# Kernel optimization log

Measured on AMD Instinct MI355X. Metric: run time of the kernel, lower is better.

## Reference

```python
import jax, jax.numpy as jnp
import numpy as np

N_MICS = 8
REF_MIC = 0
DIAG_LOAD = 1e-5
PI_ITERS = 30  # power-iteration steps for principal eigenvector of Phi_nn^-1 Phi_ss


def setup_inputs() -> dict:
    key = jax.random.key(0)
    k1, k2, k3, k4 = jax.random.split(key, 4)
    B, M, F, T = 8, N_MICS, 257, 2000
    return {
        "spec_re": jax.random.normal(k1, (B, M, F, T), dtype=jnp.float32),
        "spec_im": jax.random.normal(k2, (B, M, F, T), dtype=jnp.float32),
        "speech_mask": jax.random.uniform(k3, (B, F, T), dtype=jnp.float32),
        "noise_mask": jax.random.uniform(k4, (B, F, T), dtype=jnp.float32),
    }


def _mvdr(spec_re, spec_im, speech_mask, noise_mask):
    # (B, M, F, T) complex STFT -> (B, F, M, T) for per-(batch, freq) processing
    Y = (spec_re + 1j * spec_im).astype(jnp.complex64)
    Y = jnp.transpose(Y, (0, 2, 1, 3))  # (B, F, M, T)
    M = Y.shape[2]

    def masked_cov(mask):  # mask: (B, F, T) real
        msum = mask.sum(-1) + 1e-8                       # (B, F)
        Yw = Y * mask[:, :, None, :]                      # (B, F, M, T)
        Phi = jnp.einsum('bfmt,bfnt->bfmn', Yw, Y.conj())  # (B, F, M, M)
        return Phi / msum[..., None, None]

    Phi_ss = masked_cov(speech_mask)
    eye = jnp.eye(M, dtype=jnp.complex64)
    Phi_nn = masked_cov(noise_mask) + DIAG_LOAD * eye

    Phi_nn_inv = jnp.linalg.inv(Phi_nn)                   # batched (B, F, M, M)
    G = jnp.einsum('bfmn,bfnk->bfmk', Phi_nn_inv, Phi_ss)

    # Principal eigenvector of G via power iteration (G has real, nonnegative
    # eigenvalues since it is similar to a Hermitian-PSD generalized pencil),
    # matching torch.linalg.eig + argmax(eigenvalues.real) up to scale.
    v = jnp.ones(G.shape[:-1], dtype=jnp.complex64)       # (B, F, M)
    for _ in range(PI_ITERS):
        v = jnp.einsum('bfmn,bfn->bfm', G, v)
        v = v / (jnp.linalg.norm(v, axis=-1, keepdims=True) + 1e-12)

    # Relative transfer function normalized to reference mic (removes scale)
    rtf = v / (v[..., REF_MIC:REF_MIC + 1] + 1e-8)        # (B, F, M)

    d = jnp.einsum('bfmn,bfn->bfm', Phi_nn_inv, rtf)      # Phi_nn^-1 rtf
    denom = jnp.einsum('bfm,bfm->bf', rtf.conj(), d).real + 1e-8
    w = d / denom[..., None]                              # (B, F, M) MVDR weights

    enhanced = jnp.einsum('bfm,bfmt->bft', w.conj(), Y)   # (B, F, T) complex
    return enhanced


def reference(spec_re, spec_im, speech_mask, noise_mask):
    return _mvdr(spec_re, spec_im, speech_mask, noise_mask)
```

## Files before the change

### kernel.cpp

```cpp
#include <hip/hip_runtime.h>

#define B_DIM 8
#define M_MICS 8
#define F_DIM 257
#define T_DIM 2000


#define PAIR_ACC(mq, nq, k)                                             \
    {                                                                   \
        const float pr = yr[mq][u] * yr[nq][u] + yi[mq][u] * yi[nq][u]; \
        const float pi = yi[mq][u] * yr[nq][u] - yr[mq][u] * yi[nq][u]; \
        acc[(k) + 0] += msv[u] * pr;                                    \
        acc[(k) + 1] += msv[u] * pi;                                    \
        acc[(k) + 2] += mnv[u] * pr;                                    \
        acc[(k) + 3] += mnv[u] * pi;                                    \
    }

__launch_bounds__(256, 4)
__global__ void mvdr_fused(const float* __restrict__ sre, const float* __restrict__ sim,
                           const float* __restrict__ smask, const float* __restrict__ nmask,
                           float* __restrict__ out, int out_mode)
{
    const int f = blockIdx.x, b = blockIdx.y, tid = threadIdx.x;
    const int h = tid >> 6, l = tid & 63;

    __shared__ float sG[4][34];
    __shared__ float sW[16];

    const size_t mrow = (size_t)F_DIM * T_DIM;
    const size_t base_bf = ((size_t)(b * M_MICS) * F_DIM + f) * T_DIM;
    const size_t mbase   = ((size_t)b * F_DIM + f) * T_DIM;

    float acc[34];
#pragma unroll
    for (int i = 0; i < 34; ++i) acc[i] = 0.f;

#pragma unroll 1
    for (int it = 0; it < 16; ++it) {
        const int t0 = 2 * l + 128 * it;
        if (t0 < T_DIM) {
            float yr[8][2], yi[8][2];
#pragma unroll
            for (int m = 0; m < 8; ++m) {
                const float2 vr = *reinterpret_cast<const float2*>(sre + base_bf + (size_t)m * mrow + t0);
                const float2 vi = *reinterpret_cast<const float2*>(sim + base_bf + (size_t)m * mrow + t0);
                yr[m][0] = vr.x; yr[m][1] = vr.y;
                yi[m][0] = vi.x; yi[m][1] = vi.y;
            }
            const float2 ms2 = *reinterpret_cast<const float2*>(smask + mbase + t0);
            const float2 mn2 = *reinterpret_cast<const float2*>(nmask + mbase + t0);
            const float msv[2] = { ms2.x, ms2.y };
            const float mnv[2] = { mn2.x, mn2.y };

            if (h == 0) {
#pragma unroll
                for (int u = 0; u < 2; ++u) {
                    acc[0] += msv[u];
                    acc[1] += mnv[u];
#pragma unroll
                    for (int m = 0; m < 8; ++m) {
                        const float pd = yr[m][u] * yr[m][u] + yi[m][u] * yi[m][u];
                        acc[2 + m]  += msv[u] * pd;
                        acc[10 + m] += mnv[u] * pd;
                    }
                    PAIR_ACC(0, 1, 18) PAIR_ACC(0, 2, 22) PAIR_ACC(0, 3, 26) PAIR_ACC(0, 4, 30)
                }
            } else if (h == 1) {
#pragma unroll
                for (int u = 0; u < 2; ++u) {
                    PAIR_ACC(0, 5, 0)  PAIR_ACC(0, 6, 4)  PAIR_ACC(0, 7, 8)  PAIR_ACC(1, 2, 12)
                    PAIR_ACC(1, 3, 16) PAIR_ACC(1, 4, 20) PAIR_ACC(1, 5, 24) PAIR_ACC(1, 6, 28)
                }
            } else if (h == 2) {
#pragma unroll
                for (int u = 0; u < 2; ++u) {
                    PAIR_ACC(1, 7, 0)  PAIR_ACC(2, 3, 4)  PAIR_ACC(2, 4, 8)  PAIR_ACC(2, 5, 12)
                    PAIR_ACC(2, 6, 16) PAIR_ACC(2, 7, 20) PAIR_ACC(3, 4, 24) PAIR_ACC(3, 5, 28)
                }
            } else {
#pragma unroll
                for (int u = 0; u < 2; ++u) {
                    PAIR_ACC(3, 6, 0)  PAIR_ACC(3, 7, 4)  PAIR_ACC(4, 5, 8)  PAIR_ACC(4, 6, 12)
                    PAIR_ACC(4, 7, 16) PAIR_ACC(5, 6, 20) PAIR_ACC(5, 7, 24) PAIR_ACC(6, 7, 28)
                }
            }
        }
    }

#pragma unroll
    for (int i = 0; i < 34; ++i) {
        acc[i] += __shfl_xor(acc[i], 1, 64);
        acc[i] += __shfl_xor(acc[i], 2, 64);
        acc[i] += __shfl_xor(acc[i], 4, 64);
        acc[i] += __shfl_xor(acc[i], 8, 64);
        acc[i] += __shfl_xor(acc[i], 16, 64);
        acc[i] += __shfl_xor(acc[i], 32, 64);
    }
    if (l == 0) {
#pragma unroll
        for (int i = 0; i < 34; ++i) sG[h][i] = acc[i];
    }
    __syncthreads();

    if (tid < 64) {
        const int r = tid >> 3, cc = tid & 7;
        const float Ssum = sG[0][0] + 1e-8f;
        const float Nsum = sG[0][1] + 1e-8f;

        float ssr, ssi, ar, ai;
        if (r == cc) {
            ssr = sG[0][2 + r] / Ssum;  ssi = 0.f;
            ar  = sG[0][10 + r] / Nsum + 1e-5f;  ai = 0.f;
        } else {
            const int mm  = (r < cc) ? r : cc;
            const int nn2 = (r < cc) ? cc : r;
            const int q = mm * 8 - mm * (mm + 1) / 2 + nn2 - mm - 1;
            const int g = (q < 4) ? 0 : (1 + ((q - 4) >> 3));
            const int basei = (q < 4) ? (18 + 4 * q) : (4 * ((q - 4) & 7));
            const float sgn = (r < cc) ? 1.f : -1.f;
            ssr = sG[g][basei] / Ssum;
            ssi = sgn * sG[g][basei + 1] / Ssum;
            ar  = sG[g][basei + 2] / Nsum;
            ai  = sgn * sG[g][basei + 3] / Nsum;
        }

        float br = (r == cc) ? 1.f : 0.f, bi = 0.f;
        for (int k = 0; k < 8; ++k) {
            const float pr = __shfl(ar, k * 9, 64);
            const float pi = __shfl(ai, k * 9, 64);
            const float den = pr * pr + pi * pi;
            const float qr = pr / den, qi = -pi / den;
            const bool isk = (r == k);
            const float ar2 = ar * qr - ai * qi;
            const float ai2 = ar * qi + ai * qr;
            const float br2 = br * qr - bi * qi;
            const float bi2 = br * qi + bi * qr;
            ar = isk ? ar2 : ar; ai = isk ? ai2 : ai;
            br = isk ? br2 : br; bi = isk ? bi2 : bi;
            const float rar = __shfl(ar, k * 8 + cc, 64);
            const float rai = __shfl(ai, k * 8 + cc, 64);
            const float rbr = __shfl(br, k * 8 + cc, 64);
            const float rbi = __shfl(bi, k * 8 + cc, 64);
            const float fr = __shfl(ar, r * 8 + k, 64);
            const float fi = __shfl(ai, r * 8 + k, 64);
            const float uar = ar - (fr * rar - fi * rai);
            const float uai = ai - (fr * rai + fi * rar);
            const float ubr = br - (fr * rbr - fi * rbi);
            const float ubi = bi - (fr * rbi + fi * rbr);
            ar = isk ? ar : uar; ai = isk ? ai : uai;
            br = isk ? br : ubr; bi = isk ? bi : ubi;
        }

        float gr = 0.f, gi = 0.f;
        for (int k = 0; k < 8; ++k) {
            const float ir = __shfl(br, r * 8 + k, 64);
            const float ii = __shfl(bi, r * 8 + k, 64);
            const float skr = __shfl(ssr, k * 8 + cc, 64);
            const float ski = __shfl(ssi, k * 8 + cc, 64);
            gr += ir * skr - ii * ski;
            gi += ir * ski + ii * skr;
        }

        float vr = 1.f, vi = 0.f;
        for (int itp = 0; itp < 30; ++itp) {
            float wr2 = gr * vr - gi * vi;
            float wi2 = gr * vi + gi * vr;
            wr2 += __shfl_xor(wr2, 1, 64); wi2 += __shfl_xor(wi2, 1, 64);
            wr2 += __shfl_xor(wr2, 2, 64); wi2 += __shfl_xor(wi2, 2, 64);
            wr2 += __shfl_xor(wr2, 4, 64); wi2 += __shfl_xor(wi2, 4, 64);
            float nrm = wr2 * wr2 + wi2 * wi2;
            nrm += __shfl_xor(nrm, 8, 64);
            nrm += __shfl_xor(nrm, 16, 64);
            nrm += __shfl_xor(nrm, 32, 64);
            const float inv = 1.f / (sqrtf(nrm) + 1e-12f);
            wr2 *= inv; wi2 *= inv;
            vr = __shfl(wr2, cc * 9, 64);
            vi = __shfl(wi2, cc * 9, 64);
        }

        const float v0r = __shfl(vr, 0, 64) + 1e-8f;
        const float v0i = __shfl(vi, 0, 64);
        const float dd = v0r * v0r + v0i * v0i;
        const float rtr = (vr * v0r + vi * v0i) / dd;
        const float rti = (vi * v0r - vr * v0i) / dd;

        float dr = br * rtr - bi * rti;
        float di = br * rti + bi * rtr;
        dr += __shfl_xor(dr, 1, 64); di += __shfl_xor(di, 1, 64);
        dr += __shfl_xor(dr, 2, 64); di += __shfl_xor(di, 2, 64);
        dr += __shfl_xor(dr, 4, 64); di += __shfl_xor(di, 4, 64);

        float qden = (r == cc) ? (rtr * dr + rti * di) : 0.f;
        qden += __shfl_xor(qden, 1, 64); qden += __shfl_xor(qden, 2, 64);
        qden += __shfl_xor(qden, 4, 64); qden += __shfl_xor(qden, 8, 64);
        qden += __shfl_xor(qden, 16, 64); qden += __shfl_xor(qden, 32, 64);
        qden += 1e-8f;

        if (cc == 0) {
            sW[r]     = dr / qden;
            sW[8 + r] = di / qden;
        }
    }
    __syncthreads();

    float wr[M_MICS], wi[M_MICS];
#pragma unroll
    for (int m = 0; m < M_MICS; ++m) { wr[m] = sW[m]; wi[m] = sW[8 + m]; }

#pragma unroll 1
    for (int g = 0; g < 4; ++g) {
        const int t0 = g * 512 + 2 * tid;
        if (t0 < T_DIM) {
            float er0 = 0.f, ei0 = 0.f, er1 = 0.f, ei1 = 0.f;
#pragma unroll
            for (int m = 0; m < M_MICS; ++m) {
                const float2 vr2 = *reinterpret_cast<const float2*>(sre + base_bf + (size_t)m * mrow + t0);
                const float2 vi2 = *reinterpret_cast<const float2*>(sim + base_bf + (size_t)m * mrow + t0);
                er0 += wr[m] * vr2.x + wi[m] * vi2.x;
                ei0 += wr[m] * vi2.x - wi[m] * vr2.x;
                er1 += wr[m] * vr2.y + wi[m] * vi2.y;
                ei1 += wr[m] * vi2.y - wi[m] * vr2.y;
            }
            if (out_mode == 2) {
                *reinterpret_cast<float4*>(out + 2 * (mbase + t0)) = make_float4(er0, ei0, er1, ei1);
            } else {
                *reinterpret_cast<float2*>(out + mbase + t0) = make_float2(er0, er1);
            }
        }
    }
}

extern "C" void kernel_launch(void* const* d_in, const int* in_sizes, int n_in,
                              void* d_out, int out_size, void* d_ws, size_t ws_size,
                              hipStream_t stream)
{
    const float* sre   = (const float*)d_in[0];
    const float* sim   = (const float*)d_in[1];
    const float* smask = (const float*)d_in[2];
    const float* nmask = (const float*)d_in[3];
    float* out = (float*)d_out;

    const int mode = (out_size >= 2 * B_DIM * F_DIM * T_DIM) ? 2 : 1;

    mvdr_fused<<<dim3(F_DIM, B_DIM), 256, 0, stream>>>(sre, sim, smask, nmask, out, mode);
}
```

Measured before the change: 182.0 us.

## Split fused MVDR kernel into covariance/solve and parallel apply kernels

Splits the single fused kernel into two. The first computes the covariances, the solve and the MVDR weights, then writes the weights to a global device buffer. The second applies the weights with a grid four times wider over time chunks and declares higher occupancy. The intent is to stop the serial per-block solve from holding up the bandwidth-bound apply phase. The cost is a second launch and a second full read of the spectrum that may no longer hit cache.

```diff
diff --git a/kernel.cpp b/kernel.cpp
--- a/kernel.cpp
+++ b/kernel.cpp
@@ -4,6 +4,9 @@
 #define M_MICS 8
 #define F_DIM 257
 #define T_DIM 2000
+#define NPROB (B_DIM * F_DIM)
+
+__device__ float g_w[NPROB * 16];
 
 
 #define PAIR_ACC(mq, nq, k)                                             \
@@ -16,16 +19,14 @@
         acc[(k) + 3] += mnv[u] * pi;                                    \
     }
 
-__launch_bounds__(256, 4)
-__global__ void mvdr_fused(const float* __restrict__ sre, const float* __restrict__ sim,
-                           const float* __restrict__ smask, const float* __restrict__ nmask,
-                           float* __restrict__ out, int out_mode)
+__launch_bounds__(256, 2)
+__global__ void cov_solve_kernel(const float* __restrict__ sre, const float* __restrict__ sim,
+                                 const float* __restrict__ smask, const float* __restrict__ nmask)
 {
     const int f = blockIdx.x, b = blockIdx.y, tid = threadIdx.x;
     const int h = tid >> 6, l = tid & 63;
 
     __shared__ float sG[4][34];
-    __shared__ float sW[16];
 
     const size_t mrow = (size_t)F_DIM * T_DIM;
     const size_t base_bf = ((size_t)(b * M_MICS) * F_DIM + f) * T_DIM;
@@ -197,36 +198,46 @@
         qden += 1e-8f;
 
         if (cc == 0) {
-            sW[r]     = dr / qden;
-            sW[8 + r] = di / qden;
-        }
-    }
+            const int p = b * F_DIM + f;
+            g_w[p * 16 + r]     = dr / qden;
+            g_w[p * 16 + 8 + r] = di / qden;
+        }
+    }
+}
+
+__launch_bounds__(256, 8)
+__global__ void apply_kernel(const float* __restrict__ sre, const float* __restrict__ sim,
+                             float* __restrict__ out, int out_mode)
+{
+    const int f = blockIdx.x, b = blockIdx.y, z = blockIdx.z;
+    const int tid = threadIdx.x;
+    __shared__ float sW[16];
+    const int p = b * F_DIM + f;
+    if (tid < 16) sW[tid] = g_w[p * 16 + tid];
     __syncthreads();
 
-    float wr[M_MICS], wi[M_MICS];
-#pragma unroll
-    for (int m = 0; m < M_MICS; ++m) { wr[m] = sW[m]; wi[m] = sW[8 + m]; }
-
-#pragma unroll 1
-    for (int g = 0; g < 4; ++g) {
-        const int t0 = g * 512 + 2 * tid;
-        if (t0 < T_DIM) {
-            float er0 = 0.f, ei0 = 0.f, er1 = 0.f, ei1 = 0.f;
-#pragma unroll
-            for (int m = 0; m < M_MICS; ++m) {
-                const float2 vr2 = *reinterpret_cast<const float2*>(sre + base_bf + (size_t)m * mrow + t0);
-                const float2 vi2 = *reinterpret_cast<const float2*>(sim + base_bf + (size_t)m * mrow + t0);
-                er0 += wr[m] * vr2.x + wi[m] * vi2.x;
-                ei0 += wr[m] * vi2.x - wi[m] * vr2.x;
-                er1 += wr[m] * vr2.y + wi[m] * vi2.y;
-                ei1 += wr[m] * vi2.y - wi[m] * vr2.y;
-            }
-            if (out_mode == 2) {
-                *reinterpret_cast<float4*>(out + 2 * (mbase + t0)) = make_float4(er0, ei0, er1, ei1);
-            } else {
-                *reinterpret_cast<float2*>(out + mbase + t0) = make_float2(er0, er1);
-            }
-        }
+    const int t0 = z * 512 + 2 * tid;
+    if (t0 >= T_DIM) return;
+
+    const size_t mrow = (size_t)F_DIM * T_DIM;
+    const size_t base_bf = ((size_t)(b * M_MICS) * F_DIM + f) * T_DIM;
+    const size_t mbase   = ((size_t)b * F_DIM + f) * T_DIM;
+
+    float er0 = 0.f, ei0 = 0.f, er1 = 0.f, ei1 = 0.f;
+#pragma unroll
+    for (int m = 0; m < 8; ++m) {
+        const float2 vr2 = *reinterpret_cast<const float2*>(sre + base_bf + (size_t)m * mrow + t0);
+        const float2 vi2 = *reinterpret_cast<const float2*>(sim + base_bf + (size_t)m * mrow + t0);
+        const float wr = sW[m], wi = sW[8 + m];
+        er0 += wr * vr2.x + wi * vi2.x;
+        ei0 += wr * vi2.x - wi * vr2.x;
+        er1 += wr * vr2.y + wi * vi2.y;
+        ei1 += wr * vi2.y - wi * vr2.y;
+    }
+    if (out_mode == 2) {
+        *reinterpret_cast<float4*>(out + 2 * (mbase + t0)) = make_float4(er0, ei0, er1, ei1);
+    } else {
+        *reinterpret_cast<float2*>(out + mbase + t0) = make_float2(er0, er1);
     }
 }
 
@@ -242,5 +253,6 @@
 
     const int mode = (out_size >= 2 * B_DIM * F_DIM * T_DIM) ? 2 : 1;
 
-    mvdr_fused<<<dim3(F_DIM, B_DIM), 256, 0, stream>>>(sre, sim, smask, nmask, out, mode);
+    cov_solve_kernel<<<dim3(F_DIM, B_DIM), 256, 0, stream>>>(sre, sim, smask, nmask);
+    apply_kernel<<<dim3(F_DIM, B_DIM, 4), 256, 0, stream>>>(sre, sim, out, mode);
 }
```

New measurement: 161.1 us. 11.5% less time.
